# Kernel optimization log

Hardware: AMD Instinct MI355X
Metric: run time of the kernel (lower is better)

Reference implementation:

```python
import jax, jax.numpy as jnp
import numpy as np
import math

DN = ('NCHW', 'OIHW', 'NCHW')

def conv3x3(x, w, b):
    # 3x3, stride 1, SAME padding conv with bias, NCHW layout
    y = jax.lax.conv_general_dilated(x, w, window_strides=(1, 1), padding='SAME', dimension_numbers=DN)
    return y + b[None, :, None, None]

def setup_inputs() -> dict:
    key = jax.random.key(0)
    ks = jax.random.split(key, 12)
    B, C, NC, S = 16, 256, 80, 4  # batch, fpn channels, num_classes, stem depth
    std = 0.01
    inp = {}
    inp['feat_p3'] = jax.random.normal(ks[0], (B, C, 64, 64), jnp.float32)
    inp['feat_p4'] = jax.random.normal(ks[1], (B, C, 32, 32), jnp.float32)
    inp['feat_p5'] = jax.random.normal(ks[2], (B, C, 16, 16), jnp.float32)
    # stem conv stacks: (S, out_c, in_c, 3, 3); all channels equal so stacking is valid
    inp['stem_cls_w'] = std * jax.random.normal(ks[3], (S, C, C, 3, 3), jnp.float32)
    inp['stem_cls_b'] = jnp.zeros((S, C), jnp.float32)
    inp['stem_box_w'] = std * jax.random.normal(ks[4], (S, C, C, 3, 3), jnp.float32)
    inp['stem_box_b'] = jnp.zeros((S, C), jnp.float32)
    inp['pred_cls_w'] = std * jax.random.normal(ks[5], (NC, C, 3, 3), jnp.float32)
    inp['pred_cls_b'] = jnp.full((NC,), -math.log(99.0), jnp.float32)  # prior-prob bias init
    inp['pred_box_w'] = std * jax.random.normal(ks[6], (4, C, 3, 3), jnp.float32)
    inp['pred_box_b'] = jnp.zeros((4,), jnp.float32)
    inp['pred_ctr_w'] = std * jax.random.normal(ks[7], (1, C, 3, 3), jnp.float32)
    inp['pred_ctr_b'] = jnp.zeros((1,), jnp.float32)
    return inp

def _flatten_hw(t):
    # (B, Ch, H, W) -> (B, H*W, Ch), channels-last as in the torch module
    B, Ch, H, W = t.shape
    return t.transpose(0, 2, 3, 1).reshape(B, H * W, Ch)

def reference(feat_p3, feat_p4, feat_p5, stem_cls_w, stem_cls_b, stem_box_w, stem_box_b,
              pred_cls_w, pred_cls_b, pred_box_w, pred_box_b, pred_ctr_w, pred_ctr_b):
    per_level = []
    for feat in (feat_p3, feat_p4, feat_p5):
        cls_feat = feat
        box_feat = feat
        for i in range(stem_cls_w.shape[0]):  # fixed small stem depth (4)
            cls_feat = jax.nn.relu(conv3x3(cls_feat, stem_cls_w[i], stem_cls_b[i]))
            box_feat = jax.nn.relu(conv3x3(box_feat, stem_box_w[i], stem_box_b[i]))
        cls_logits = conv3x3(cls_feat, pred_cls_w, pred_cls_b)   # (B, 80, H, W)
        box_deltas = conv3x3(box_feat, pred_box_w, pred_box_b)   # (B, 4, H, W)
        ctr_logits = conv3x3(box_feat, pred_ctr_w, pred_ctr_b)   # (B, 1, H, W)
        per_level.append(jnp.concatenate(
            [_flatten_hw(cls_logits), _flatten_hw(box_deltas), _flatten_hw(ctr_logits)], axis=-1))
    # concat p3/p4/p5 along location axis -> (B, 4096+1024+256, 85)
    return jnp.concatenate(per_level, axis=1)
```

## Files before the change

kernel.cpp:

```cpp
#include <hip/hip_runtime.h>


typedef __bf16 bf16;
typedef __attribute__((ext_vector_type(8))) __bf16 bf16x8;
typedef __attribute__((ext_vector_type(4))) float f32x4;

typedef unsigned int uint32_as1 __attribute__((address_space(1)));
typedef unsigned int uint32_as3 __attribute__((address_space(3)));

__device__ __forceinline__ void gl_lds16(const bf16* g, bf16* l) {
    __builtin_amdgcn_global_load_lds(
        (const uint32_as1*)(unsigned long long)g,
        (uint32_as3*)(unsigned int)(unsigned long long)l,
        16, 0, 0);
}

struct StemTab {
    const bf16* inC[3]; const bf16* inB[3];
    bf16* outC[3]; bf16* outB[3];
    int H[3]; int lw[3]; int lhw[3];
    int xend0, xend1;
};
struct PredTab {
    const bf16* inC[3]; const bf16* inB[3];
    int H[3]; int lw[3]; int lhw[3]; int offl[3];
    int xend0, xend1;
};
struct CastTab {
    const float* in[3]; bf16* out[3];
    int H[3]; int lw[3];
    int xend0, xend1;
};
struct BZTab {
    bf16* base[3]; int H[3]; size_t bufE[3]; int ppi[3];
    int xend0, xend1;
};

__global__ __launch_bounds__(256) void stem_conv_kernel(
    StemTab tab, const bf16* __restrict__ Wc, const bf16* __restrict__ Wb,
    const float* __restrict__ bc, const float* __restrict__ bb)
{
    const int bx = blockIdx.x;
    const int l  = (bx >= tab.xend0) + (bx >= tab.xend1);
    const int start = (l == 0) ? 0 : (l == 1 ? tab.xend0 : tab.xend1);
    const int local = bx - start;
    const int H = tab.H[l], lw = tab.lw[l], lhw = tab.lhw[l];

    const bf16* A; bf16* O; const bf16* BT; const float* bias;
    if (blockIdx.z == 0) { A = tab.inC[l]; O = tab.outC[l]; BT = Wc; bias = bc; }
    else                 { A = tab.inB[l]; O = tab.outB[l]; BT = Wb; bias = bb; }

    const int W   = 1 << lw;
    const int Wp  = W + 2;
    const int HW  = 1 << lhw;
    const int tid = threadIdx.x;
    const int m_base = (local >> 1) * 128;
    const int n0     = (local & 1) * 128;
    const int b   = m_base >> lhw;
    const int y0  = (m_base & (HW - 1)) >> lw;
    const int ibase = b * (H + 2) * Wp * 256;

    __shared__ __align__(16) bf16 Sh[18432];
    bf16* Als = Sh;
    bf16* Bls = Sh + 10240;

    const int ch8   = (((tid & 7) ^ ((tid >> 3) & 7)) << 3);
    const int rbase = tid >> 3;
    const int Wp256 = Wp * 256;
    const int npx   = (128 >> lw) * Wp;
    const int toff  = (128 + rbase < npx) ? 4 * 8192 : 0;
    const int ag0   = ibase + rbase * 256 + ch8;
    int bg[4];
#pragma unroll
    for (int i = 0; i < 4; ++i)
        bg[i] = (n0 + i * 32 + rbase) * 256 + ch8;

    f32x4 acc[4][4];
#pragma unroll
    for (int i = 0; i < 4; ++i)
#pragma unroll
        for (int j = 0; j < 4; ++j)
            acc[i][j] = (f32x4)(0.0f);

    const int lane = tid & 63;
    const int wv   = tid >> 6;
    const int wm   = (wv & 1) * 64;
    const int wn   = (wv >> 1) * 64;
    const int l16  = lane & 15;
    const int quad = lane >> 4;
    int pb[4];
#pragma unroll
    for (int i = 0; i < 4; ++i) {
        const int mm = wm + i * 16;
        pb[i] = mm + ((mm >> lw) << 1) + l16;
    }
    const int bRow = (wn + l16) * 64;
    const int bsw  = l16 & 7;
    bf16* lA = Als + tid * 8;
    bf16* lB = Bls + tid * 8;

    for (int dy = 0; dy < 3; ++dy) {
        const int abase = ag0 + (y0 + dy) * Wp256;
        for (int cq = 0; cq < 4; ++cq) {
            const int c0 = cq << 6;
#pragma unroll
            for (int i = 0; i < 4; ++i)
                gl_lds16(A + abase + c0 + i * 8192, lA + i * 2048);
            gl_lds16(A + abase + c0 + toff, lA + 4 * 2048);
            for (int dx = 0; dx < 3; ++dx) {
                const int boff = (dy * 3 + dx) * 65536 + c0;
#pragma unroll
                for (int i = 0; i < 4; ++i)
                    gl_lds16(BT + bg[i] + boff, lB + i * 2048);
                __syncthreads();
                int rowi[4];
#pragma unroll
                for (int i = 0; i < 4; ++i) rowi[i] = pb[i] + dx;
#pragma unroll
                for (int ks = 0; ks < 2; ++ks) {
                    const int qk = quad + ks * 4;
                    bf16x8 af[4], bfv[4];
#pragma unroll
                    for (int i = 0; i < 4; ++i)
                        af[i] = *(const bf16x8*)(Als + (rowi[i] << 6) +
                                                 ((qk ^ (rowi[i] & 7)) << 3));
#pragma unroll
                    for (int j = 0; j < 4; ++j)
                        bfv[j] = *(const bf16x8*)(Bls + bRow + j * 1024 +
                                                  ((qk ^ bsw) << 3));
#pragma unroll
                    for (int i = 0; i < 4; ++i)
#pragma unroll
                        for (int j = 0; j < 4; ++j)
                            acc[i][j] = __builtin_amdgcn_mfma_f32_16x16x32_bf16(
                                af[i], bfv[j], acc[i][j], 0, 0, 0);
                }
                __syncthreads();
            }
        }
    }

    float bv[4];
#pragma unroll
    for (int j = 0; j < 4; ++j) bv[j] = bias[n0 + wn + j * 16 + l16];
    bf16* Tw = Sh + wv * 4096;
#pragma unroll
    for (int i = 0; i < 4; ++i)
#pragma unroll
        for (int r = 0; r < 4; ++r) {
            const int row = i * 16 + quad * 4 + r;
#pragma unroll
            for (int j = 0; j < 4; ++j) {
                float v = acc[i][j][r] + bv[j];
                v = v > 0.0f ? v : 0.0f;
                const int sc = (((j * 2 + (l16 >> 3)) ^ (row & 7)) << 3) + (l16 & 7);
                Tw[row * 64 + sc] = (bf16)v;
            }
        }
    __syncthreads();
    const int rgrp = lane >> 3, cc = lane & 7;
#pragma unroll
    for (int p = 0; p < 8; ++p) {
        const int row = p * 8 + rgrp;
        bf16x8 vv = *(const bf16x8*)(Tw + row * 64 + ((cc ^ (row & 7)) << 3));
        const int ml = wm + row;
        const int y  = y0 + (ml >> lw);
        const int x  = ml & (W - 1);
        *(bf16x8*)(O + ibase + ((y + 1) * Wp + (x + 1)) * 256 + n0 + wn + cc * 8) = vv;
    }
}

__global__ __launch_bounds__(256) void pred_conv_kernel(
    PredTab tab, const bf16* __restrict__ BT, const float* __restrict__ bias,
    float* __restrict__ out)
{
    const int bx = blockIdx.x;
    const int l  = (bx >= tab.xend0) + (bx >= tab.xend1);
    const int start = (l == 0) ? 0 : (l == 1 ? tab.xend0 : tab.xend1);
    const int mt = bx - start;
    const int H = tab.H[l], lw = tab.lw[l], lhw = tab.lhw[l], off_l = tab.offl[l];
    const bf16* Ac = tab.inC[l];
    const bf16* Ab = tab.inB[l];

    const int W   = 1 << lw;
    const int Wp  = W + 2;
    const int HW  = 1 << lhw;
    const int tid = threadIdx.x;
    const int m_base = mt * 128;
    const int b   = m_base >> lhw;
    const int mi  = m_base & (HW - 1);
    const int y0  = mi >> lw;
    const int ibase = b * (H + 2) * Wp * 256;

    __shared__ __align__(16) bf16 Sh[(128 + 128 + 96) * 64];

    const int ch8   = (((tid & 7) ^ ((tid >> 3) & 7)) << 3);
    const int rbase = tid >> 3;
    int ag[4], bg[3];
#pragma unroll
    for (int i = 0; i < 4; ++i) {
        int row = i * 32 + rbase;
        int y = y0 + (row >> lw);
        int x = row & (W - 1);
        ag[i] = ibase + (y * Wp + x) * 256 + ch8;
    }
#pragma unroll
    for (int i = 0; i < 3; ++i)
        bg[i] = (i * 32 + rbase) * 256 + ch8;

    f32x4 accC[2][5], accB[2];
#pragma unroll
    for (int i = 0; i < 2; ++i) {
#pragma unroll
        for (int j = 0; j < 5; ++j) accC[i][j] = (f32x4)(0.0f);
        accB[i] = (f32x4)(0.0f);
    }

    const int lane = tid & 63;
    const int wv   = tid >> 6;
    const int l16  = lane & 15;
    const int quad = lane >> 4;
    const int xsw  = l16 & 7;
    const int aRow = (wv * 32 + l16) * 64;
    bf16* lS = Sh + tid * 8;

    for (int kc = 0; kc < 36; ++kc) {
        const int t  = kc >> 2;
        const int dy = t / 3;
        const int dx = t - dy * 3;
        const int c0 = (kc & 3) << 6;
        const int aoff = (dy * Wp + dx) * 256 + c0;
        const int boff = t * 24576 + c0;
#pragma unroll
        for (int i = 0; i < 4; ++i)
            gl_lds16(Ac + ag[i] + aoff, lS + i * 2048);
#pragma unroll
        for (int i = 0; i < 4; ++i)
            gl_lds16(Ab + ag[i] + aoff, lS + (4 + i) * 2048);
#pragma unroll
        for (int i = 0; i < 3; ++i)
            gl_lds16(BT + bg[i] + boff, lS + (8 + i) * 2048);
        __syncthreads();
#pragma unroll
        for (int ks = 0; ks < 2; ++ks) {
            const int cO = (((quad + ks * 4) ^ xsw) << 3);
            bf16x8 afc[2], afb[2], bfv[5], bfb;
#pragma unroll
            for (int i = 0; i < 2; ++i) {
                afc[i] = *(const bf16x8*)(Sh + aRow + i * 1024 + cO);
                afb[i] = *(const bf16x8*)(Sh + 8192 + aRow + i * 1024 + cO);
            }
#pragma unroll
            for (int j = 0; j < 5; ++j)
                bfv[j] = *(const bf16x8*)(Sh + 16384 + (j * 16 + l16) * 64 + cO);
            bfb = *(const bf16x8*)(Sh + 16384 + (80 + l16) * 64 + cO);
#pragma unroll
            for (int i = 0; i < 2; ++i) {
#pragma unroll
                for (int j = 0; j < 5; ++j)
                    accC[i][j] = __builtin_amdgcn_mfma_f32_16x16x32_bf16(
                        afc[i], bfv[j], accC[i][j], 0, 0, 0);
                accB[i] = __builtin_amdgcn_mfma_f32_16x16x32_bf16(
                    afb[i], bfb, accB[i], 0, 0, 0);
            }
        }
        __syncthreads();
    }

#pragma unroll
    for (int i = 0; i < 2; ++i) {
#pragma unroll
        for (int r = 0; r < 4; ++r) {
            const int ml  = wv * 32 + i * 16 + quad * 4 + r;
            const int pos = mi + ml;
            const int ob  = (b * 5376 + off_l + pos) * 85;
#pragma unroll
            for (int j = 0; j < 5; ++j)
                out[ob + j * 16 + l16] = accC[i][j][r] + bias[j * 16 + l16];
            if (l16 < 5)
                out[ob + 80 + l16] = accB[i][r] + bias[80 + l16];
        }
    }
}

__global__ __launch_bounds__(256) void cast_pad_kernel(CastTab tb)
{
    const int bx = blockIdx.x;
    const int l  = (bx >= tb.xend0) + (bx >= tb.xend1);
    const int start = (l == 0) ? 0 : (l == 1 ? tb.xend0 : tb.xend1);
    const int job = bx - start;
    const int H = tb.H[l], lw = tb.lw[l];
    const int W = 1 << lw, Wp = W + 2;
    const int b = job >> lw;
    const int y = job & (W - 1);
    const float* in = tb.in[l] + ((size_t)(b * 256) * H + y) * W;
    bf16* out = tb.out[l] + ((size_t)(b * (H + 2) + y + 1) * Wp + 1) * 256;
    const int tid = threadIdx.x;
    __shared__ bf16 L[16384];
    const int cpp = 256 >> lw;
    const int x = tid & (W - 1);
    const int cb0 = tid >> lw;
    for (int p = 0; p < W; ++p) {
        const int c = p * cpp + cb0;
        float v = in[(size_t)c * H * W + x];
        L[x * 256 + ((((c >> 3) ^ (x & 31))) << 3) + (c & 7)] = (bf16)v;
    }
    __syncthreads();
    const int wpass = W >> 3;
    for (int q = 0; q < wpass; ++q) {
        const int id = q * 256 + tid;
        const int xo = id >> 5;
        const int k  = id & 31;
        bf16x8 vv = *(const bf16x8*)(L + xo * 256 + ((k ^ (xo & 31)) << 3));
        *(bf16x8*)(out + xo * 256 + k * 8) = vv;
    }
}

__global__ void border_zero_kernel(BZTab tb)
{
    const int bx = blockIdx.x;
    const int l  = (bx >= tb.xend0) + (bx >= tb.xend1);
    const int start = (l == 0) ? 0 : (l == 1 ? tb.xend0 : tb.xend1);
    const int i   = bx - start;
    const int buf = blockIdx.y;
    const int c   = threadIdx.x;
    const int H = tb.H[l];
    const int ppi = tb.ppi[l];
    const int img = i / ppi;
    const int p   = i - img * ppi;
    const int Wp  = H + 2, Hp = H + 2;
    int y, xp;
    if (p < Wp)            { y = 0;      xp = p; }
    else if (p < 2 * Wp)   { y = Hp - 1; xp = p - Wp; }
    else { int q = p - 2 * Wp; y = 1 + (q >> 1); xp = (q & 1) ? (Wp - 1) : 0; }
    tb.base[l][buf * tb.bufE[l] + ((size_t)(img * Hp + y) * Wp + xp) * 256 + c]
        = (bf16)0.0f;
}

__global__ void prepack_kernel(const float* __restrict__ scw,
                               const float* __restrict__ sbw,
                               const float* __restrict__ pcw,
                               const float* __restrict__ pbw,
                               const float* __restrict__ prw,
                               const float* __restrict__ pcb,
                               const float* __restrict__ pbb,
                               const float* __restrict__ prb,
                               bf16* __restrict__ wc, bf16* __restrict__ wb,
                               bf16* __restrict__ pT, float* __restrict__ pB)
{
    const int ci = threadIdx.x;
    int g = blockIdx.x;
    if (g < 18432) {
        const float* w = (g < 9216) ? scw : sbw;
        bf16* o        = (g < 9216) ? wc  : wb;
        if (g >= 9216) g -= 9216;
        const int co = g & 255;
        const int st = g >> 8;
        const int s  = st / 9;
        const int t  = st - s * 9;
        o[(size_t)g * 256 + ci] = (bf16)w[(((s * 256 + co) * 256 + ci) * 9) + t];
    } else {
        g -= 18432;
        const int t  = g / 96;
        const int co = g - t * 96;
        float v = 0.0f;
        if (co < 80)       v = pcw[((co * 256 + ci) * 9) + t];
        else if (co < 84)  v = pbw[(((co - 80) * 256 + ci) * 9) + t];
        else if (co == 84) v = prw[(ci * 9) + t];
        pT[(size_t)g * 256 + ci] = (bf16)v;
        if (g == 0 && ci < 96) {
            float bvv = 0.0f;
            if (ci < 80)       bvv = pcb[ci];
            else if (ci < 84)  bvv = pbb[ci - 80];
            else if (ci == 84) bvv = prb[0];
            pB[ci] = bvv;
        }
    }
}

extern "C" void kernel_launch(void* const* d_in, const int* in_sizes, int n_in,
                              void* d_out, int out_size, void* d_ws, size_t ws_size,
                              hipStream_t stream)
{
    (void)in_sizes; (void)n_in; (void)out_size;
    const float* feat[3] = {(const float*)d_in[0], (const float*)d_in[1],
                            (const float*)d_in[2]};
    const float* scw = (const float*)d_in[3];
    const float* scb = (const float*)d_in[4];
    const float* sbw = (const float*)d_in[5];
    const float* sbb = (const float*)d_in[6];
    const float* pcw = (const float*)d_in[7];
    const float* pcb = (const float*)d_in[8];
    const float* pbw = (const float*)d_in[9];
    const float* pbb = (const float*)d_in[10];
    const float* prw = (const float*)d_in[11];
    const float* prb = (const float*)d_in[12];
    float* out = (float*)d_out;

    const int Hs[3]   = {64, 32, 16};
    const int lws[3]  = {6, 5, 4};
    const int lhws[3] = {12, 10, 8};
    const int offl[3] = {0, 4096, 5120};
    const int mtiles[3] = {512, 128, 32};
    size_t bufB[3];
    for (int l = 0; l < 3; ++l)
        bufB[l] = (size_t)16 * (Hs[l] + 2) * (Hs[l] + 2) * 256 * 2;

    const size_t WSTEM = (size_t)4 * 9 * 256 * 256 * 2;
    const size_t WPRED = (size_t)9 * 96 * 256 * 2;
    const size_t FULL   = 5 * (bufB[0] + bufB[1] + bufB[2]) + 2 * WSTEM + WPRED + 384;
    const size_t SHARED = 5 * bufB[0] + 2 * WSTEM + WPRED + 384;
    if (ws_size < SHARED) return;
    const bool fused = ws_size >= FULL;

    char* ws = (char*)d_ws;
    bf16* act[3][5];
    size_t off = 0;
    if (fused) {
        for (int l = 0; l < 3; ++l)
            for (int k = 0; k < 5; ++k) { act[l][k] = (bf16*)(ws + off); off += bufB[l]; }
    } else {
        for (int k = 0; k < 5; ++k)
            for (int l = 0; l < 3; ++l) act[l][k] = (bf16*)(ws + (size_t)k * bufB[0]);
        off = 5 * bufB[0];
    }
    bf16*  wbTc = (bf16*)(ws + off); off += WSTEM;
    bf16*  wbTb = (bf16*)(ws + off); off += WSTEM;
    bf16*  pT   = (bf16*)(ws + off); off += WPRED;
    float* pB   = (float*)(ws + off);

    prepack_kernel<<<dim3(19296), 256, 0, stream>>>(scw, sbw, pcw, pbw, prw,
                                                    pcb, pbb, prb,
                                                    wbTc, wbTb, pT, pB);

    auto make_stem_tab = [&](int s, int nlev, const int* levs) {
        StemTab tb{};
        for (int i = 0; i < nlev; ++i) {
            int l = levs[i];
            tb.inC[i]  = (s == 0) ? act[l][0] : ((s & 1) ? act[l][1] : act[l][2]);
            tb.inB[i]  = (s == 0) ? act[l][0] : ((s & 1) ? act[l][3] : act[l][4]);
            tb.outC[i] = (s & 1) ? act[l][2] : act[l][1];
            tb.outB[i] = (s & 1) ? act[l][4] : act[l][3];
            tb.H[i] = Hs[l]; tb.lw[i] = lws[l]; tb.lhw[i] = lhws[l];
        }
        return tb;
    };

    if (fused) {
        BZTab bz{};
        int bpx[3];
        for (int l = 0; l < 3; ++l) {
            bz.base[l] = act[l][0]; bz.H[l] = Hs[l]; bz.bufE[l] = bufB[l] / 2;
            bpx[l] = 2 * (Hs[l] + 2) + 2 * Hs[l];
            bz.ppi[l] = bpx[l];
        }
        bz.xend0 = 16 * bpx[0]; bz.xend1 = bz.xend0 + 16 * bpx[1];
        const int bztot = bz.xend1 + 16 * bpx[2];
        border_zero_kernel<<<dim3(bztot, 5), 256, 0, stream>>>(bz);

        CastTab ct{};
        for (int l = 0; l < 3; ++l) {
            ct.in[l] = feat[l]; ct.out[l] = act[l][0];
            ct.H[l] = Hs[l]; ct.lw[l] = lws[l];
        }
        ct.xend0 = 16 * Hs[0]; ct.xend1 = ct.xend0 + 16 * Hs[1];
        cast_pad_kernel<<<dim3(ct.xend1 + 16 * Hs[2]), 256, 0, stream>>>(ct);

        const int levs[3] = {0, 1, 2};
        const int tx0 = mtiles[0] * 2, tx1 = mtiles[1] * 2, tx2 = mtiles[2] * 2;
        for (int s = 0; s < 4; ++s) {
            StemTab tb = make_stem_tab(s, 3, levs);
            tb.xend0 = tx0; tb.xend1 = tx0 + tx1;
            stem_conv_kernel<<<dim3(tx0 + tx1 + tx2, 1, 2), 256, 0, stream>>>(
                tb, wbTc + (size_t)s * 589824, wbTb + (size_t)s * 589824,
                scb + s * 256, sbb + s * 256);
        }
        PredTab pt{};
        for (int l = 0; l < 3; ++l) {
            pt.inC[l] = act[l][2]; pt.inB[l] = act[l][4];
            pt.H[l] = Hs[l]; pt.lw[l] = lws[l]; pt.lhw[l] = lhws[l]; pt.offl[l] = offl[l];
        }
        pt.xend0 = mtiles[0]; pt.xend1 = mtiles[0] + mtiles[1];
        pred_conv_kernel<<<dim3(mtiles[0] + mtiles[1] + mtiles[2]), 256, 0, stream>>>(
            pt, pT, pB, out);
    } else {
        for (int l = 0; l < 3; ++l) {
            const int bpx = 2 * (Hs[l] + 2) + 2 * Hs[l];
            BZTab bz{};
            bz.base[0] = act[l][0]; bz.H[0] = Hs[l]; bz.bufE[0] = bufB[0] / 2;
            bz.ppi[0] = bpx; bz.xend0 = 16 * bpx; bz.xend1 = 16 * bpx;
            border_zero_kernel<<<dim3(16 * bpx, 5), 256, 0, stream>>>(bz);
            CastTab ct{};
            ct.in[0] = feat[l]; ct.out[0] = act[l][0];
            ct.H[0] = Hs[l]; ct.lw[0] = lws[l];
            ct.xend0 = 16 * Hs[l]; ct.xend1 = 16 * Hs[l];
            cast_pad_kernel<<<dim3(16 * Hs[l]), 256, 0, stream>>>(ct);

            const int levs[1] = {l};
            const int tiles = mtiles[l] * 2;
            for (int s = 0; s < 4; ++s) {
                StemTab tb = make_stem_tab(s, 1, levs);
                tb.xend0 = tiles; tb.xend1 = tiles;
                stem_conv_kernel<<<dim3(tiles, 1, 2), 256, 0, stream>>>(
                    tb, wbTc + (size_t)s * 589824, wbTb + (size_t)s * 589824,
                    scb + s * 256, sbb + s * 256);
            }
            PredTab pt{};
            pt.inC[0] = act[l][2]; pt.inB[0] = act[l][4];
            pt.H[0] = Hs[l]; pt.lw[0] = lws[l]; pt.lhw[0] = lhws[l]; pt.offl[0] = offl[l];
            pt.xend0 = mtiles[l]; pt.xend1 = mtiles[l];
            pred_conv_kernel<<<dim3(mtiles[l]), 256, 0, stream>>>(pt, pT, pB, out);
        }
    }
}
```

Before: 992.7 us.

## Double-buffer A and B LDS tiles in stem conv to overlap loads with MFMA

Grows shared memory and splits it into two A buffers and two B buffers. The global-to-LDS loads for the next (dy, cq, dx) step are now issued before the current step's MFMA work, and one of the two barriers per step is dropped. The aim is to hide global load latency behind compute. The cost is roughly double the LDS footprint (about 68KB), which may lower occupancy. The tail-row load also changes, from a thread-dependent offset to a fixed row offset.

```diff
diff --git a/kernel.cpp b/kernel.cpp
--- a/kernel.cpp
+++ b/kernel.cpp
@@ -60,15 +60,13 @@
     const int y0  = (m_base & (HW - 1)) >> lw;
     const int ibase = b * (H + 2) * Wp * 256;
 
-    __shared__ __align__(16) bf16 Sh[18432];
-    bf16* Als = Sh;
-    bf16* Bls = Sh + 10240;
+    __shared__ __align__(16) bf16 Sh[34816];
 
     const int ch8   = (((tid & 7) ^ ((tid >> 3) & 7)) << 3);
     const int rbase = tid >> 3;
     const int Wp256 = Wp * 256;
     const int npx   = (128 >> lw) * Wp;
-    const int toff  = (128 + rbase < npx) ? 4 * 8192 : 0;
+    const int trow  = (npx - 25) & ~7;
     const int ag0   = ibase + rbase * 256 + ch8;
     int bg[4];
 #pragma unroll
@@ -96,37 +94,57 @@
     }
     const int bRow = (wn + l16) * 64;
     const int bsw  = l16 & 7;
-    bf16* lA = Als + tid * 8;
-    bf16* lB = Bls + tid * 8;
-
-    for (int dy = 0; dy < 3; ++dy) {
-        const int abase = ag0 + (y0 + dy) * Wp256;
-        for (int cq = 0; cq < 4; ++cq) {
-            const int c0 = cq << 6;
-#pragma unroll
-            for (int i = 0; i < 4; ++i)
-                gl_lds16(A + abase + c0 + i * 8192, lA + i * 2048);
-            gl_lds16(A + abase + c0 + toff, lA + 4 * 2048);
+
+    bf16* const lA = Sh + tid * 8;
+    bf16* const lB = Sh + 18432 + tid * 8;
+
+    auto stageA = [&](int ab, int dy, int cq) {
+        const bf16* src = A + ag0 + (y0 + dy) * Wp256 + (cq << 6);
+        bf16* dst = lA + ab * 9216;
+#pragma unroll
+        for (int i = 0; i < 4; ++i)
+            gl_lds16(src + i * 8192, dst + i * 2048);
+        gl_lds16(src + trow * 256, dst + trow * 64);
+    };
+    auto stageB = [&](int bb, int dy, int cq, int dx) {
+        const int boff = (dy * 3 + dx) * 65536 + (cq << 6);
+        bf16* dst = lB + bb * 8192;
+#pragma unroll
+        for (int i = 0; i < 4; ++i)
+            gl_lds16(BT + bg[i] + boff, dst + i * 2048);
+    };
+
+    stageA(0, 0, 0);
+    stageB(0, 0, 0, 0);
+    __syncthreads();
+
+    int cura = 0, curb = 0;
+    for (int dy = 0; dy < 3; ++dy)
+        for (int cq = 0; cq < 4; ++cq)
+#pragma unroll
             for (int dx = 0; dx < 3; ++dx) {
-                const int boff = (dy * 3 + dx) * 65536 + c0;
-#pragma unroll
-                for (int i = 0; i < 4; ++i)
-                    gl_lds16(BT + bg[i] + boff, lB + i * 2048);
-                __syncthreads();
-                int rowi[4];
-#pragma unroll
-                for (int i = 0; i < 4; ++i) rowi[i] = pb[i] + dx;
+                int ndy = dy, ncq = cq, ndx = dx + 1;
+                if (ndx == 3) { ndx = 0; if (++ncq == 4) { ncq = 0; ++ndy; } }
+                const bool more = (ndy < 3);
+                if (more) {
+                    if (ndx == 0) stageA(cura ^ 1, ndy, ncq);
+                    stageB(curb ^ 1, ndy, ncq, ndx);
+                }
+                const bf16* Ac_ = Sh + cura * 9216;
+                const bf16* Bc_ = Sh + 18432 + curb * 8192;
 #pragma unroll
                 for (int ks = 0; ks < 2; ++ks) {
                     const int qk = quad + ks * 4;
                     bf16x8 af[4], bfv[4];
 #pragma unroll
-                    for (int i = 0; i < 4; ++i)
-                        af[i] = *(const bf16x8*)(Als + (rowi[i] << 6) +
-                                                 ((qk ^ (rowi[i] & 7)) << 3));
+                    for (int i = 0; i < 4; ++i) {
+                        const int ri = pb[i] + dx;
+                        af[i] = *(const bf16x8*)(Ac_ + (ri << 6) +
+                                                 ((qk ^ (ri & 7)) << 3));
+                    }
 #pragma unroll
                     for (int j = 0; j < 4; ++j)
-                        bfv[j] = *(const bf16x8*)(Bls + bRow + j * 1024 +
+                        bfv[j] = *(const bf16x8*)(Bc_ + bRow + j * 1024 +
                                                   ((qk ^ bsw) << 3));
 #pragma unroll
                     for (int i = 0; i < 4; ++i)
@@ -136,9 +154,8 @@
                                 af[i], bfv[j], acc[i][j], 0, 0, 0);
                 }
                 __syncthreads();
+                if (more) { curb ^= 1; if (ndx == 0) cura ^= 1; }
             }
-        }
-    }
 
     float bv[4];
 #pragma unroll
```

New measurement: 1.365 ms. 37.5% more time.

## Double-buffer stem conv weight tiles in LDS with prefetch of next tap

Applied to the files above, without the earlier changes.

Grows LDS to hold two B weight buffers and prefetches the next tap's weight tile via global_load_lds while the current tap's MFMAs run. The fixed __syncthreads is replaced by an explicit vmcnt wait plus s_barrier. This is meant to hide global load latency for the weights. The cost is higher LDS use, which may reduce occupancy. Correctness depends on the vmcnt(4) count matching the outstanding loads, including the A loads issued at each cq step.

```diff
diff --git a/kernel.cpp b/kernel.cpp
--- a/kernel.cpp
+++ b/kernel.cpp
@@ -60,7 +60,7 @@
     const int y0  = (m_base & (HW - 1)) >> lw;
     const int ibase = b * (H + 2) * Wp * 256;
 
-    __shared__ __align__(16) bf16 Sh[18432];
+    __shared__ __align__(16) bf16 Sh[26624];
     bf16* Als = Sh;
     bf16* Bls = Sh + 10240;
 
@@ -96,23 +96,44 @@
     }
     const int bRow = (wn + l16) * 64;
     const int bsw  = l16 & 7;
-    bf16* lA = Als + tid * 8;
-    bf16* lB = Bls + tid * 8;
-
-    for (int dy = 0; dy < 3; ++dy) {
-        const int abase = ag0 + (y0 + dy) * Wp256;
+    bf16* const lA = Als + tid * 8;
+    bf16* const lB = Bls + tid * 8;
+
+    auto stageA = [&](int dy, int cq) {
+        const int abase = ag0 + (y0 + dy) * Wp256 + (cq << 6);
+#pragma unroll
+        for (int i = 0; i < 4; ++i)
+            gl_lds16(A + abase + i * 8192, lA + i * 2048);
+        gl_lds16(A + abase + toff, lA + 4 * 2048);
+    };
+    auto stageB = [&](int half, int tap, int cq) {
+        const int boff = tap * 65536 + (cq << 6);
+        bf16* dst = lB + half * 8192;
+#pragma unroll
+        for (int i = 0; i < 4; ++i)
+            gl_lds16(BT + bg[i] + boff, dst + i * 2048);
+    };
+
+    stageB(0, 0, 0);
+    int curb = 0;
+
+    for (int dy = 0; dy < 3; ++dy)
         for (int cq = 0; cq < 4; ++cq) {
-            const int c0 = cq << 6;
-#pragma unroll
-            for (int i = 0; i < 4; ++i)
-                gl_lds16(A + abase + c0 + i * 8192, lA + i * 2048);
-            gl_lds16(A + abase + c0 + toff, lA + 4 * 2048);
+            stageA(dy, cq);
+#pragma unroll
             for (int dx = 0; dx < 3; ++dx) {
-                const int boff = (dy * 3 + dx) * 65536 + c0;
-#pragma unroll
-                for (int i = 0; i < 4; ++i)
-                    gl_lds16(BT + bg[i] + boff, lB + i * 2048);
-                __syncthreads();
+                int ndy = dy, ncq = cq, ndx = dx + 1;
+                if (ndx == 3) { ndx = 0; if (++ncq == 4) { ncq = 0; ++ndy; } }
+                const bool more = (ndy < 3);
+                if (more) {
+                    stageB(curb ^ 1, ndy * 3 + ndx, ncq);
+                    asm volatile("s_waitcnt vmcnt(4)" ::: "memory");
+                } else {
+                    asm volatile("s_waitcnt vmcnt(0)" ::: "memory");
+                }
+                __builtin_amdgcn_s_barrier();
+                __builtin_amdgcn_sched_barrier(0);
+                const bf16* Bc = Bls + curb * 8192;
                 int rowi[4];
 #pragma unroll
                 for (int i = 0; i < 4; ++i) rowi[i] = pb[i] + dx;
@@ -126,7 +147,7 @@
                                                  ((qk ^ (rowi[i] & 7)) << 3));
 #pragma unroll
                     for (int j = 0; j < 4; ++j)
-                        bfv[j] = *(const bf16x8*)(Bls + bRow + j * 1024 +
+                        bfv[j] = *(const bf16x8*)(Bc + bRow + j * 1024 +
                                                   ((qk ^ bsw) << 3));
 #pragma unroll
                     for (int i = 0; i < 4; ++i)
@@ -135,10 +156,11 @@
                             acc[i][j] = __builtin_amdgcn_mfma_f32_16x16x32_bf16(
                                 af[i], bfv[j], acc[i][j], 0, 0, 0);
                 }
-                __syncthreads();
+                __builtin_amdgcn_sched_barrier(0);
+                __builtin_amdgcn_s_barrier();
+                curb ^= 1;
             }
         }
-    }
 
     float bv[4];
 #pragma unroll
```

Measured after the change: 1.032 ms. 3.9% more time.

## Reuse padded input row tile across dx taps in prediction conv kernel

Applied to the files above, without the earlier changes.

Restructures the prediction-head implicit-GEMM loop so each dy/channel-quarter loads a contiguous padded span of input rows (including halo pixels) into LDS once. The three dx taps then index into it with shifted row offsets instead of reloading the A tiles per tap, cutting global-to-LDS traffic for activations to about a third. The price is a larger LDS buffer with per-row swizzle arithmetic, an extra tail load, and more syncs per A load, since only B is reloaded for each dx.

```diff
diff --git a/kernel.cpp b/kernel.cpp
--- a/kernel.cpp
+++ b/kernel.cpp
@@ -192,18 +192,15 @@
     const int y0  = mi >> lw;
     const int ibase = b * (H + 2) * Wp * 256;
 
-    __shared__ __align__(16) bf16 Sh[(128 + 128 + 96) * 64];
+    __shared__ __align__(16) bf16 Sh[24576];
 
     const int ch8   = (((tid & 7) ^ ((tid >> 3) & 7)) << 3);
     const int rbase = tid >> 3;
-    int ag[4], bg[3];
-#pragma unroll
-    for (int i = 0; i < 4; ++i) {
-        int row = i * 32 + rbase;
-        int y = y0 + (row >> lw);
-        int x = row & (W - 1);
-        ag[i] = ibase + (y * Wp + x) * 256 + ch8;
-    }
+    const int Wp256 = Wp * 256;
+    const int npx   = (128 >> lw) * Wp;
+    const int trow  = (npx - 25) & ~7;
+    const int ag0   = ibase + rbase * 256 + ch8;
+    int bg[3];
 #pragma unroll
     for (int i = 0; i < 3; ++i)
         bg[i] = (i * 32 + rbase) * 256 + ch8;
@@ -220,51 +217,67 @@
     const int wv   = tid >> 6;
     const int l16  = lane & 15;
     const int quad = lane >> 4;
-    const int xsw  = l16 & 7;
-    const int aRow = (wv * 32 + l16) * 64;
-    bf16* lS = Sh + tid * 8;
-
-    for (int kc = 0; kc < 36; ++kc) {
-        const int t  = kc >> 2;
-        const int dy = t / 3;
-        const int dx = t - dy * 3;
-        const int c0 = (kc & 3) << 6;
-        const int aoff = (dy * Wp + dx) * 256 + c0;
-        const int boff = t * 24576 + c0;
-#pragma unroll
-        for (int i = 0; i < 4; ++i)
-            gl_lds16(Ac + ag[i] + aoff, lS + i * 2048);
-#pragma unroll
-        for (int i = 0; i < 4; ++i)
-            gl_lds16(Ab + ag[i] + aoff, lS + (4 + i) * 2048);
-#pragma unroll
-        for (int i = 0; i < 3; ++i)
-            gl_lds16(BT + bg[i] + boff, lS + (8 + i) * 2048);
-        __syncthreads();
-#pragma unroll
-        for (int ks = 0; ks < 2; ++ks) {
-            const int cO = (((quad + ks * 4) ^ xsw) << 3);
-            bf16x8 afc[2], afb[2], bfv[5], bfb;
-#pragma unroll
-            for (int i = 0; i < 2; ++i) {
-                afc[i] = *(const bf16x8*)(Sh + aRow + i * 1024 + cO);
-                afb[i] = *(const bf16x8*)(Sh + 8192 + aRow + i * 1024 + cO);
+    int pbp[2];
+#pragma unroll
+    for (int i = 0; i < 2; ++i) {
+        const int mm = wv * 32 + i * 16;
+        pbp[i] = mm + ((mm >> lw) << 1) + l16;
+    }
+    const int bsw = l16 & 7;
+    bf16* const lAc = Sh + tid * 8;
+    bf16* const lAb = Sh + 9216 + tid * 8;
+    bf16* const lB  = Sh + 18432 + tid * 8;
+    bf16* const lAcT = Sh + trow * 64 + tid * 8;
+    bf16* const lAbT = Sh + 9216 + trow * 64 + tid * 8;
+
+    for (int dy = 0; dy < 3; ++dy) {
+        for (int cq = 0; cq < 4; ++cq) {
+            const int abase = ag0 + (y0 + dy) * Wp256 + (cq << 6);
+#pragma unroll
+            for (int i = 0; i < 4; ++i) {
+                gl_lds16(Ac + abase + i * 8192, lAc + i * 2048);
+                gl_lds16(Ab + abase + i * 8192, lAb + i * 2048);
             }
-#pragma unroll
-            for (int j = 0; j < 5; ++j)
-                bfv[j] = *(const bf16x8*)(Sh + 16384 + (j * 16 + l16) * 64 + cO);
-            bfb = *(const bf16x8*)(Sh + 16384 + (80 + l16) * 64 + cO);
-#pragma unroll
-            for (int i = 0; i < 2; ++i) {
-#pragma unroll
-                for (int j = 0; j < 5; ++j)
-                    accC[i][j] = __builtin_amdgcn_mfma_f32_16x16x32_bf16(
-                        afc[i], bfv[j], accC[i][j], 0, 0, 0);
-                accB[i] = __builtin_amdgcn_mfma_f32_16x16x32_bf16(
-                    afb[i], bfb, accB[i], 0, 0, 0);
+            gl_lds16(Ac + abase + trow * 256, lAcT);
+            gl_lds16(Ab + abase + trow * 256, lAbT);
+            for (int dx = 0; dx < 3; ++dx) {
+                const int boff = (dy * 3 + dx) * 24576 + (cq << 6);
+#pragma unroll
+                for (int i = 0; i < 3; ++i)
+                    gl_lds16(BT + bg[i] + boff, lB + i * 2048);
+                __syncthreads();
+                int rowi[2];
+#pragma unroll
+                for (int i = 0; i < 2; ++i) rowi[i] = pbp[i] + dx;
+#pragma unroll
+                for (int ks = 0; ks < 2; ++ks) {
+                    const int qk = quad + ks * 4;
+                    bf16x8 afc[2], afb[2], bfv[5], bfb;
+#pragma unroll
+                    for (int i = 0; i < 2; ++i) {
+                        const int sw = ((qk ^ (rowi[i] & 7)) << 3);
+                        afc[i] = *(const bf16x8*)(Sh + (rowi[i] << 6) + sw);
+                        afb[i] = *(const bf16x8*)(Sh + 9216 + (rowi[i] << 6) + sw);
+                    }
+                    const int cO = ((qk ^ bsw) << 3);
+#pragma unroll
+                    for (int j = 0; j < 5; ++j)
+                        bfv[j] = *(const bf16x8*)(Sh + 18432 +
+                                                  (j * 16 + l16) * 64 + cO);
+                    bfb = *(const bf16x8*)(Sh + 18432 + (80 + l16) * 64 + cO);
+#pragma unroll
+                    for (int i = 0; i < 2; ++i) {
+#pragma unroll
+                        for (int j = 0; j < 5; ++j)
+                            accC[i][j] = __builtin_amdgcn_mfma_f32_16x16x32_bf16(
+                                afc[i], bfv[j], accC[i][j], 0, 0, 0);
+                        accB[i] = __builtin_amdgcn_mfma_f32_16x16x32_bf16(
+                            afb[i], bfb, accB[i], 0, 0, 0);
+                    }
+                }
+                __syncthreads();
             }
         }
-        __syncthreads();
     }
 
 #pragma unroll
```

Result: faster. 936.1 us (-5.7%).
